# Kernel tuning notes

Measured on AMD Instinct MI355X. Metric: run time of the kernel, lower is better.

Reference implementation:

```python
import jax, jax.numpy as jnp
import numpy as np

B, L, E, H, T = 8, 4096, 512, 8, 2
D = E // H


def setup_inputs() -> dict:
    key = jax.random.key(0)
    ks = jax.random.split(key, 11)
    s = 0.02
    return {
        "query": jax.random.normal(ks[0], (B, L, E), jnp.float32),
        "key": jax.random.normal(ks[1], (B, L, E), jnp.float32),
        "value": jax.random.normal(ks[2], (B, L, E), jnp.float32),
        "Wq": jax.random.normal(ks[3], (T, E, E), jnp.float32) * s,
        "bq": jax.random.normal(ks[4], (T, E), jnp.float32) * s,
        "Wk": jax.random.normal(ks[5], (T, E, E), jnp.float32) * s,
        "bk": jax.random.normal(ks[6], (T, E), jnp.float32) * s,
        "Wv": jax.random.normal(ks[7], (E, E), jnp.float32) * s,
        "bv": jax.random.normal(ks[8], (E,), jnp.float32) * s,
        "Wout": jax.random.normal(ks[9], (E, E), jnp.float32) * s,
        "bout": jax.random.normal(ks[10], (E,), jnp.float32) * s,
    }


def reference(query, key, value, Wq, bq, Wk, bk, Wv, bv, Wout, bout):
    bsz, tgt_len, embed_dim = query.shape
    src_len = key.shape[1]
    n_head = H
    head_dim = embed_dim // n_head

    # value projection: (B,S,H,D)
    v = (value @ Wv.T + bv).reshape(bsz, src_len, n_head, head_dim)
    # faithful to torch: value.view(-1, bsz*n_head, head_dim).transpose(0,1)
    # WITHOUT permuting to (S,B,H,D) first -> pure memory reinterpretation
    v = jnp.swapaxes(v.reshape(src_len, bsz * n_head, head_dim), 0, 1)  # (BH,S,D)

    # per-term q/k projections -> (T,L,B,H,D) / (T,S,B,H,D)
    q = jnp.einsum('ble,tfe->tblf', query, Wq) + bq[:, None, None, :]
    k = jnp.einsum('bse,tfe->tbsf', key, Wk) + bk[:, None, None, :]
    q = q.reshape(T, bsz, tgt_len, n_head, head_dim).transpose(0, 2, 1, 3, 4)
    k = k.reshape(T, bsz, src_len, n_head, head_dim).transpose(0, 2, 1, 3, 4)

    # act_fun == softmax: q softmax over feature dim, k softmax over sequence dim (dim 0)
    q = jax.nn.softmax(q, axis=-1)
    k = jax.nn.softmax(k, axis=1)

    # flatten: (T, L, B*H, D) -> (T, B*H, L, D)
    q = jnp.swapaxes(q.reshape(T, tgt_len, bsz * n_head, head_dim), 1, 2)
    k = jnp.swapaxes(k.reshape(T, src_len, bsz * n_head, head_dim), 1, 2)

    # cosine positional reweighting (cosFormer): doubles feature dim
    m = max(src_len, tgt_len)
    idx = (np.pi / 2) * jnp.arange(1, m + 1, dtype=q.dtype) / m  # (m,)
    sin_q = jnp.sin(idx[:tgt_len])[None, None, :, None]
    cos_q = jnp.cos(idx[:tgt_len])[None, None, :, None]
    sin_k = jnp.sin(idx[:src_len])[None, None, :, None]
    cos_k = jnp.cos(idx[:src_len])[None, None, :, None]
    q = jnp.concatenate([q * sin_q, q * cos_q], axis=-1)  # (T,BH,L,2D)
    k = jnp.concatenate([k * sin_k, k * cos_k], axis=-1)  # (T,BH,S,2D)

    # linear attention: kv state then output, summed over terms
    kv = jnp.einsum('tnsd,nsm->tndm', k, v)          # (T,BH,2D,D)
    out = jnp.einsum('tnld,tndm->nlm', q, kv)        # (BH,L,D) summed over T

    # back to (B,L,E)
    out = jnp.swapaxes(out, 0, 1).reshape(tgt_len, bsz, embed_dim)
    out = jnp.swapaxes(out, 0, 1)
    return out @ Wout.T + bout
```

## Files before the change

### kernel.cpp

```cpp
#include <hip/hip_runtime.h>
#include <cstdio>

#define E_DIM 512
#define L_DIM 4096
#define B_DIM 8
#define H_DIM 8
#define T_DIM 2
#define M_ROWS 32768

typedef __attribute__((ext_vector_type(8))) __bf16 bf16x8;
typedef __attribute__((ext_vector_type(4))) float f32x4;

static __device__ __forceinline__ unsigned short f2bf(float f) {
  unsigned int u = __float_as_uint(f);
  return (unsigned short)((u + 0x7FFFu + ((u >> 16) & 1u)) >> 16);
}
static __device__ __forceinline__ unsigned int pkbf(float lo, float hi) {
  return (unsigned int)f2bf(lo) | ((unsigned int)f2bf(hi) << 16);
}
static __device__ __forceinline__ float bf2f(unsigned short u) {
  return __uint_as_float((unsigned int)u << 16);
}
static __device__ __forceinline__ void unpk8(uint4 u, float* f) {
  f[0] = bf2f((unsigned short)u.x); f[1] = bf2f((unsigned short)(u.x >> 16));
  f[2] = bf2f((unsigned short)u.y); f[3] = bf2f((unsigned short)(u.y >> 16));
  f[4] = bf2f((unsigned short)u.z); f[5] = bf2f((unsigned short)(u.z >> 16));
  f[6] = bf2f((unsigned short)u.w); f[7] = bf2f((unsigned short)(u.w >> 16));
}
static __device__ __forceinline__ int swz64(int row, int e) {
  return row * 64 + ((((e >> 3) ^ row) & 7) << 3) + (e & 7);
}
static __device__ __forceinline__ int swz128(int row, int e) {
  return row * 128 + ((((e >> 3) ^ row) & 7) << 3) + ((e >> 3) & 8) * 8 + (e & 7);
}
static __device__ __forceinline__ void gl_lds16(const unsigned short* g,
                                                unsigned short* l) {
  __builtin_amdgcn_global_load_lds(
      (const __attribute__((address_space(1))) unsigned int*)g,
      (__attribute__((address_space(3))) unsigned int*)l, 16, 0, 0);
}

__global__ void sincos_kernel(float* __restrict__ sintab, float* __restrict__ costab) {
  int i = blockIdx.x * blockDim.x + threadIdx.x;
  if (i < L_DIM) {
    float idx = 1.57079632679489662f * (float)(i + 1) / (float)L_DIM;
    sintab[i] = sinf(idx);
    costab[i] = cosf(idx);
  }
}

__global__ void convf2b(const float* __restrict__ src, unsigned short* __restrict__ dst,
                        int n8) {
  for (int i = blockIdx.x * blockDim.x + threadIdx.x; i < n8; i += gridDim.x * blockDim.x) {
    float4 a = *(const float4*)(src + (size_t)i * 8);
    float4 b = *(const float4*)(src + (size_t)i * 8 + 4);
    uint4 o;
    o.x = pkbf(a.x, a.y); o.y = pkbf(a.z, a.w);
    o.z = pkbf(b.x, b.y); o.w = pkbf(b.z, b.w);
    *(uint4*)(dst + (size_t)i * 8) = o;
  }
}

#define YHALF 16777216
template <bool OUTF32, bool STATS, int NBL2>
__global__ __launch_bounds__(256) void gemm_xwt(
    const unsigned short* __restrict__ X, const unsigned short* __restrict__ W,
    const float* __restrict__ bias, void* __restrict__ Yv,
    float* __restrict__ pmax, float* __restrict__ psum) {
  __shared__ __align__(16) unsigned short smem[32768];
  const int tid = threadIdx.x;
  const int id = blockIdx.x;
  const int j = id >> 3;
  const int mb = (id & 7) * 32 + (j >> NBL2);
  const int nb = j & ((1 << NBL2) - 1);
  const int m0 = mb * 128, n0 = nb * 128;
  const int lane = tid & 63;
  const int w = tid >> 6;
  const int wr = w >> 1, wc = w & 1;
  const int lr = lane & 15;
  const int lk = (lane >> 4) * 8;
  const int rq = lane >> 4;
  const int srow = lane >> 3;
  const int gsrc8 = ((lane & 7) ^ srow) * 8;
  f32x4 acc[4][4];
#pragma unroll
  for (int i = 0; i < 4; ++i)
#pragma unroll
    for (int jj = 0; jj < 4; ++jj) acc[i][jj] = (f32x4){0.f, 0.f, 0.f, 0.f};

#pragma unroll
  for (int i = 0; i < 4; ++i) {
    int rb = w * 32 + i * 8;
    gl_lds16(X + (size_t)(m0 + rb + srow) * 512 + gsrc8, &smem[rb * 64]);
    gl_lds16(W + (size_t)(n0 + rb + srow) * 512 + gsrc8, &smem[8192 + rb * 64]);
  }
  __syncthreads();

#pragma unroll
  for (int step = 0; step < 8; ++step) {
    const int cur = step & 1;
    if (step < 7) {
      unsigned short* Ab = smem + (cur ^ 1) * 16384;
      const int kn = (step + 1) * 64;
#pragma unroll
      for (int i = 0; i < 4; ++i) {
        int rb = w * 32 + i * 8;
        gl_lds16(X + (size_t)(m0 + rb + srow) * 512 + kn + gsrc8, &Ab[rb * 64]);
        gl_lds16(W + (size_t)(n0 + rb + srow) * 512 + kn + gsrc8,
                 &Ab[8192 + rb * 64]);
      }
    }
    const unsigned short* As = smem + cur * 16384;
    const unsigned short* Bs = As + 8192;
#pragma unroll
    for (int kk = 0; kk < 2; ++kk) {
      bf16x8 av[4], bv[4];
      int ke = kk * 32 + lk;
#pragma unroll
      for (int fm = 0; fm < 4; ++fm)
        av[fm] = *(const bf16x8*)&As[swz64(wr * 64 + fm * 16 + lr, ke)];
#pragma unroll
      for (int fn = 0; fn < 4; ++fn)
        bv[fn] = *(const bf16x8*)&Bs[swz64(wc * 64 + fn * 16 + lr, ke)];
#pragma unroll
      for (int fm = 0; fm < 4; ++fm)
#pragma unroll
        for (int fn = 0; fn < 4; ++fn)
          acc[fm][fn] = __builtin_amdgcn_mfma_f32_16x16x32_bf16(av[fm], bv[fn],
                                                                acc[fm][fn], 0, 0, 0);
    }
    __syncthreads();
  }

  if (STATS) {
    float* sf = (float*)smem;
#pragma unroll
    for (int fn = 0; fn < 4; ++fn) {
      float M = -3.0e38f;
#pragma unroll
      for (int fm = 0; fm < 4; ++fm)
#pragma unroll
        for (int jj = 0; jj < 4; ++jj) M = fmaxf(M, acc[fm][fn][jj]);
      M = fmaxf(M, __shfl_xor(M, 16));
      M = fmaxf(M, __shfl_xor(M, 32));
      float S = 0.f;
#pragma unroll
      for (int fm = 0; fm < 4; ++fm)
#pragma unroll
        for (int jj = 0; jj < 4; ++jj) S += __expf(acc[fm][fn][jj] - M);
      S += __shfl_xor(S, 16);
      S += __shfl_xor(S, 32);
      if (rq == 0) {
        int col = wc * 64 + fn * 16 + lr;
        sf[wr * 128 + col] = M;
        sf[256 + wr * 128 + col] = S;
      }
    }
    __syncthreads();
    if (tid < 128) {
      float M0 = sf[tid], M1 = sf[128 + tid];
      float S0 = sf[256 + tid], S1 = sf[384 + tid];
      float nm = fmaxf(M0, M1);
      float S = S0 * __expf(M0 - nm) + S1 * __expf(M1 - nm);
      int gc = n0 + tid;
      size_t mtile = (size_t)(m0 >> 7);
      pmax[mtile * (128 << NBL2) + gc] = nm + bias[gc];
      psum[mtile * (128 << NBL2) + gc] = S;
    }
    __syncthreads();
  }

  if (!OUTF32) {
    unsigned short* Cs = smem;
#pragma unroll
    for (int fn = 0; fn < 4; ++fn) {
      int col = wc * 64 + fn * 16 + lr;
      float bb = bias[n0 + col];
#pragma unroll
      for (int fm = 0; fm < 4; ++fm) {
        int row = wr * 64 + fm * 16 + rq * 4;
#pragma unroll
        for (int jj = 0; jj < 4; ++jj)
          Cs[(row + jj) * 136 + col] = f2bf(acc[fm][fn][jj] + bb);
      }
    }
    __syncthreads();
    unsigned short* Yb = (unsigned short*)Yv + (size_t)(n0 >> 9) * YHALF;
    const int nc = n0 & 511;
#pragma unroll
    for (int i = 0; i < 8; ++i) {
      int idx = tid + i * 256;
      int row = idx >> 4, g = idx & 15;
      *(uint4*)(Yb + (size_t)(m0 + row) * 512 + nc + g * 8) =
          *(const uint4*)&Cs[row * 136 + g * 8];
    }
  } else {
    float* Cf = (float*)smem;
    float* Yf = (float*)Yv;
#pragma unroll
    for (int p = 0; p < 2; ++p) {
      if (p) __syncthreads();
      if (wr == p) {
#pragma unroll
        for (int fn = 0; fn < 4; ++fn) {
          int col = wc * 64 + fn * 16 + lr;
          float bb = bias[n0 + col];
#pragma unroll
          for (int fm = 0; fm < 4; ++fm) {
            int lrow = fm * 16 + rq * 4;
#pragma unroll
            for (int jj = 0; jj < 4; ++jj)
              Cf[(lrow + jj) * 132 + col] = acc[fm][fn][jj] + bb;
          }
        }
      }
      __syncthreads();
#pragma unroll
      for (int i = 0; i < 8; ++i) {
        int idx = tid + i * 256;
        int row = idx >> 5, g = idx & 31;
        *(float4*)(Yf + (size_t)(m0 + p * 64 + row) * 512 + n0 + g * 4) =
            *(const float4*)&Cf[row * 132 + g * 4];
      }
    }
  }
}

__global__ void kcolstats_reduce(const float* __restrict__ pmax,
                                 const float* __restrict__ psum,
                                 float* __restrict__ colmax,
                                 float* __restrict__ colinv, int coloff) {
  int i = blockIdx.x * 256 + threadIdx.x;
  int b = i >> 9, f = i & 511;
  float M = -3.0e38f, S = 0.f;
#pragma unroll
  for (int c = 0; c < 32; ++c) {
    size_t mt = (size_t)(b * 32 + c);
    float m = pmax[mt * 1024 + coloff + f];
    float s = psum[mt * 1024 + coloff + f];
    float nm = fmaxf(M, m);
    S = S * __expf(M - nm) + s * __expf(m - nm);
    M = nm;
  }
  colmax[i] = M;
  colinv[i] = 1.f / S;
}

__global__ __launch_bounds__(256) void kv_mfma(
    const unsigned short* __restrict__ Kp, const unsigned short* __restrict__ Vpb,
    const float* __restrict__ colmax, const float* __restrict__ colinv,
    const float* __restrict__ sintab, const float* __restrict__ costab,
    float* __restrict__ kvpart) {
  __shared__ __align__(16) unsigned short kT[64 * 64];
  __shared__ __align__(16) unsigned short vT[128 * 64];
  __shared__ float cmaxs[64], cinvs[64];
  const int tid = threadIdx.x;
  const int chunk = blockIdx.x;
  const int n = blockIdx.y;
  const int b = n >> 3, h = n & 7;
  if (tid < 64) {
    cmaxs[tid] = colmax[b * E_DIM + h * 64 + tid];
    cinvs[tid] = colinv[b * E_DIM + h * 64 + tid];
  }
  const int lane = tid & 63;
  const int w = tid >> 6;
  const int lr = lane & 15;
  const int lk = (lane >> 4) * 8;
  const int sp = tid & 31;
  const int g = tid >> 5;
  f32x4 acc[4][2];
#pragma unroll
  for (int i = 0; i < 4; ++i) {
    acc[i][0] = (f32x4){0.f, 0.f, 0.f, 0.f};
    acc[i][1] = (f32x4){0.f, 0.f, 0.f, 0.f};
  }
  __syncthreads();

  for (int st = 0; st < 8; ++st) {
    int sA = chunk * 512 + st * 64 + 2 * sp;
    const unsigned short* kp = Kp + ((size_t)b * L_DIM + sA) * 512 + h * 64 + g * 8;
    uint4 ka = *(const uint4*)kp;
    uint4 kb = *(const uint4*)(kp + 512);
    int vr = ((sA >> 9) << 12) + ((sA & 511) << 3) + b;
    const unsigned short* vp = Vpb + (size_t)vr * 512 + h * 64 + g * 8;
    uint4 v0 = *(const uint4*)vp;
    uint4 v1 = *(const uint4*)(vp + 8 * 512);
    float kfa[8], kfb[8], vA[8], vB[8];
    unpk8(ka, kfa);
    unpk8(kb, kfb);
    unpk8(v0, vA);
    unpk8(v1, vB);
    float sS = sintab[sA], sC = costab[sA];
    float tS = sintab[sA + 1], tC = costab[sA + 1];
    __syncthreads();
#pragma unroll
    for (int i = 0; i < 8; ++i) {
      int d = g * 8 + i;
      float e0 = __expf(kfa[i] - cmaxs[d]) * cinvs[d];
      float e1 = __expf(kfb[i] - cmaxs[d]) * cinvs[d];
      *(unsigned int*)&kT[swz64(d, 2 * sp)] = pkbf(e0, e1);
    }
#pragma unroll
    for (int i = 0; i < 8; ++i) {
      int m = g * 8 + i;
      *(unsigned int*)&vT[swz64(m, 2 * sp)] = pkbf(vA[i] * sS, vB[i] * tS);
      *(unsigned int*)&vT[swz64(64 + m, 2 * sp)] = pkbf(vA[i] * sC, vB[i] * tC);
    }
    __syncthreads();
#pragma unroll
    for (int kk = 0; kk < 2; ++kk) {
      int ke = kk * 32 + lk;
      bf16x8 av[4], bv[2];
#pragma unroll
      for (int fm = 0; fm < 4; ++fm)
        av[fm] = *(const bf16x8*)&kT[swz64(fm * 16 + lr, ke)];
#pragma unroll
      for (int fn = 0; fn < 2; ++fn)
        bv[fn] = *(const bf16x8*)&vT[swz64(w * 32 + fn * 16 + lr, ke)];
#pragma unroll
      for (int fm = 0; fm < 4; ++fm)
#pragma unroll
        for (int fn = 0; fn < 2; ++fn)
          acc[fm][fn] = __builtin_amdgcn_mfma_f32_16x16x32_bf16(av[fm], bv[fn],
                                                                acc[fm][fn], 0, 0, 0);
    }
  }
  const int rq = lane >> 4;
#pragma unroll
  for (int fn = 0; fn < 2; ++fn) {
    int ncol = w * 32 + fn * 16 + lr;
    int m = ncol & 63;
    int ddbase = (ncol >> 6) * 64;
#pragma unroll
    for (int fm = 0; fm < 4; ++fm) {
#pragma unroll
      for (int jj = 0; jj < 4; ++jj) {
        int dd = ddbase + fm * 16 + rq * 4 + jj;
        kvpart[(((size_t)chunk * 64 + n) * 64 + m) * 128 + dd] = acc[fm][fn][jj];
      }
    }
  }
}

__global__ void kv_reduce_swz(const float* __restrict__ part,
                              unsigned short* __restrict__ kvT) {
  int i = blockIdx.x * 256 + threadIdx.x;
  float s = 0.f;
#pragma unroll
  for (int c = 0; c < 8; ++c) s += part[(size_t)c * 524288 + i];
  int dd = i & 127;
  int m = (i >> 7) & 63;
  int nm = i >> 7;
  int gg = dd >> 3;
  int e = ((gg & 8) | ((gg ^ m) & 7)) * 8 + (dd & 7);
  kvT[(size_t)nm * 128 + e] = f2bf(s);
}

__global__ __launch_bounds__(256) void out_fused(
    const unsigned short* __restrict__ Qp0, const unsigned short* __restrict__ Qp1,
    const unsigned short* __restrict__ kvT,
    const float* __restrict__ sintab, const float* __restrict__ costab,
    unsigned short* __restrict__ Yb) {
  __shared__ __align__(16) unsigned short q2s[64 * 128];
  __shared__ __align__(16) unsigned short kvs[2][64 * 128];
  const int tid = threadIdx.x;
  const int lc = blockIdx.x;
  const int n = blockIdx.y;
  const int b = n >> 3, h = n & 7;
  const int lane = tid & 63;
  const int w = tid >> 6;
  {
    const uint4* s0 = (const uint4*)(kvT + (size_t)n * 8192);
    const uint4* s1 = (const uint4*)(kvT + 524288 + (size_t)n * 8192);
    uint4* d0 = (uint4*)kvs[0];
    uint4* d1 = (uint4*)kvs[1];
#pragma unroll
    for (int i = 0; i < 4; ++i) {
      d0[tid + i * 256] = s0[tid + i * 256];
      d1[tid + i * 256] = s1[tid + i * 256];
    }
  }
  const int l0 = lc * 64;
  const int wr = w >> 1, wc = w & 1;
  const int lr = lane & 15;
  const int lk = (lane >> 4) * 8;
  const int rq = lane >> 4;
  f32x4 acc[2][2];
  acc[0][0] = acc[0][1] = acc[1][0] = acc[1][1] = (f32x4){0.f, 0.f, 0.f, 0.f};
#pragma unroll
  for (int t = 0; t < 2; ++t) {
    const unsigned short* Qp = t ? Qp1 : Qp0;
    if (t) __syncthreads();
#pragma unroll
    for (int i = 0; i < 2; ++i) {
      int idx = tid + i * 256;
      int row = idx >> 3;
      int g = idx & 7;
      uint4 q = *(const uint4*)(Qp + ((size_t)b * L_DIM + l0 + row) * 512 +
                                h * 64 + g * 8);
      float v[8];
      unpk8(q, v);
      float m8 = fmaxf(fmaxf(fmaxf(v[0], v[1]), fmaxf(v[2], v[3])),
                       fmaxf(fmaxf(v[4], v[5]), fmaxf(v[6], v[7])));
      m8 = fmaxf(m8, __shfl_xor(m8, 1));
      m8 = fmaxf(m8, __shfl_xor(m8, 2));
      m8 = fmaxf(m8, __shfl_xor(m8, 4));
      float e[8], s8;
#pragma unroll
      for (int k = 0; k < 8; ++k) e[k] = __expf(v[k] - m8);
      s8 = ((e[0] + e[1]) + (e[2] + e[3])) + ((e[4] + e[5]) + (e[6] + e[7]));
      s8 += __shfl_xor(s8, 1);
      s8 += __shfl_xor(s8, 2);
      s8 += __shfl_xor(s8, 4);
      float inv = 1.f / s8;
      int gl = l0 + row;
      float sn = sintab[gl] * inv;
      float cs = costab[gl] * inv;
      uint4 os, oc;
      os.x = pkbf(e[0] * sn, e[1] * sn); os.y = pkbf(e[2] * sn, e[3] * sn);
      os.z = pkbf(e[4] * sn, e[5] * sn); os.w = pkbf(e[6] * sn, e[7] * sn);
      oc.x = pkbf(e[0] * cs, e[1] * cs); oc.y = pkbf(e[2] * cs, e[3] * cs);
      oc.z = pkbf(e[4] * cs, e[5] * cs); oc.w = pkbf(e[6] * cs, e[7] * cs);
      *(uint4*)&q2s[swz128(row, g * 8)] = os;
      *(uint4*)&q2s[swz128(row, 64 + g * 8)] = oc;
    }
    __syncthreads();
#pragma unroll
    for (int ks = 0; ks < 4; ++ks) {
      int ke = ks * 32 + lk;
      bf16x8 av[2], bv[2];
#pragma unroll
      for (int fm = 0; fm < 2; ++fm)
        av[fm] = *(const bf16x8*)&q2s[swz128(wr * 32 + fm * 16 + lr, ke)];
#pragma unroll
      for (int fn = 0; fn < 2; ++fn)
        bv[fn] = *(const bf16x8*)&kvs[t][swz128(wc * 32 + fn * 16 + lr, ke)];
#pragma unroll
      for (int fm = 0; fm < 2; ++fm)
#pragma unroll
        for (int fn = 0; fn < 2; ++fn)
          acc[fm][fn] = __builtin_amdgcn_mfma_f32_16x16x32_bf16(av[fm], bv[fn],
                                                                acc[fm][fn], 0, 0, 0);
    }
  }
  __syncthreads();
  unsigned short* Os = q2s;
#pragma unroll
  for (int fn = 0; fn < 2; ++fn) {
    int col = wc * 32 + fn * 16 + lr;
#pragma unroll
    for (int fm = 0; fm < 2; ++fm) {
      int lrow = wr * 32 + fm * 16 + rq * 4;
#pragma unroll
      for (int jj = 0; jj < 4; ++jj)
        Os[(lrow + jj) * 72 + col] = f2bf(acc[fm][fn][jj]);
    }
  }
  __syncthreads();
#pragma unroll
  for (int i = 0; i < 2; ++i) {
    int idx = tid + i * 256;
    int row = idx >> 3, g = idx & 7;
    *(uint4*)(Yb + ((size_t)b * L_DIM + l0 + row) * 512 + h * 64 + g * 8) =
        *(const uint4*)&Os[row * 72 + g * 8];
  }
}

extern "C" void kernel_launch(void* const* d_in, const int* in_sizes, int n_in,
                              void* d_out, int out_size, void* d_ws, size_t ws_size,
                              hipStream_t stream) {
  const float* query = (const float*)d_in[0];
  const float* key   = (const float*)d_in[1];
  const float* value = (const float*)d_in[2];
  const float* Wq    = (const float*)d_in[3];
  const float* bq    = (const float*)d_in[4];
  const float* Wk    = (const float*)d_in[5];
  const float* bk    = (const float*)d_in[6];
  const float* Wv    = (const float*)d_in[7];
  const float* bv    = (const float*)d_in[8];
  const float* Wout  = (const float*)d_in[9];
  const float* bout  = (const float*)d_in[10];
  float* out = (float*)d_out;
  float* ws = (float*)d_ws;

  const size_t F_PROJ0 = 0;
  const size_t F_PROJ1 = F_PROJ0 + 8388608;
  const size_t F_VPB   = F_PROJ1 + 8388608;
  const size_t F_KVP   = F_VPB + 8388608;
  const size_t F_KVT   = F_KVP + 4194304;
  const size_t F_XBUF  = F_KVT + 524288;
  const size_t F_WBF   = F_XBUF + 8388608;
  const size_t F_CMAX  = F_WBF + 786432;
  const size_t F_CINV  = F_CMAX + 8192;
  const size_t F_SIN   = F_CINV + 8192;
  const size_t F_COS   = F_SIN + 4096;
  const size_t TOTALF  = F_COS + 4096;
  if (ws_size < TOTALF * sizeof(float)) {
    fprintf(stderr, "kernel_launch: ws too small (%zu < %zu)\n", ws_size, TOTALF * 4);
    return;
  }
  unsigned short* proj0 = (unsigned short*)(ws + F_PROJ0);
  unsigned short* vpb   = (unsigned short*)(ws + F_VPB);
  float* kvpart = ws + F_KVP;
  unsigned short* kvT  = (unsigned short*)(ws + F_KVT);
  unsigned short* xbuf = (unsigned short*)(ws + F_XBUF);
  unsigned short* wbf  = (unsigned short*)(ws + F_WBF);
  float* cmax = ws + F_CMAX;
  float* cinv = ws + F_CINV;
  float* sintab = ws + F_SIN;
  float* costab = ws + F_COS;
  float* pmax = kvpart;
  float* psum = kvpart + 262144;
  const size_t WQ_O = 0, WK_O = 524288, WV_O = 1048576, WOUT_O = 1310720;

  sincos_kernel<<<16, 256, 0, stream>>>(sintab, costab);
  convf2b<<<256, 256, 0, stream>>>(Wq, wbf + WQ_O, 65536);
  convf2b<<<256, 256, 0, stream>>>(Wk, wbf + WK_O, 65536);
  convf2b<<<128, 256, 0, stream>>>(Wv, wbf + WV_O, 32768);
  convf2b<<<128, 256, 0, stream>>>(Wout, wbf + WOUT_O, 32768);

  convf2b<<<2048, 256, 0, stream>>>(value, xbuf, 2097152);
  gemm_xwt<false, false, 2><<<1024, 256, 0, stream>>>(xbuf, wbf + WV_O, bv, vpb,
                                                      nullptr, nullptr);

  convf2b<<<2048, 256, 0, stream>>>(key, xbuf, 2097152);
  gemm_xwt<false, true, 3><<<2048, 256, 0, stream>>>(xbuf, wbf + WK_O, bk, proj0,
                                                     pmax, psum);
  kcolstats_reduce<<<16, 256, 0, stream>>>(pmax, psum, cmax, cinv, 0);
  kcolstats_reduce<<<16, 256, 0, stream>>>(pmax, psum, cmax + 4096, cinv + 4096, 512);
  for (int t = 0; t < T_DIM; ++t) {
    unsigned short* projt = proj0 + (size_t)t * YHALF;
    kv_mfma<<<dim3(8, 64), 256, 0, stream>>>(projt, vpb, cmax + t * 4096,
                                             cinv + t * 4096, sintab, costab,
                                             kvpart);
    kv_reduce_swz<<<2048, 256, 0, stream>>>(kvpart, kvT + (size_t)t * 524288);
  }

  convf2b<<<2048, 256, 0, stream>>>(query, xbuf, 2097152);
  gemm_xwt<false, false, 3><<<2048, 256, 0, stream>>>(xbuf, wbf + WQ_O, bq, proj0,
                                                      nullptr, nullptr);
  out_fused<<<dim3(64, 64), 256, 0, stream>>>(proj0, proj0 + YHALF, kvT,
                                              sintab, costab, xbuf);
  gemm_xwt<true, false, 2><<<1024, 256, 0, stream>>>(xbuf, wbf + WOUT_O, bout, out,
                                                     nullptr, nullptr);
}
```

Baseline: 325.8 us.

## Fuse key softmax and KV-state accumulation into key projection GEMM epilogue

```diff
diff --git a/kernel.cpp b/kernel.cpp
--- a/kernel.cpp
+++ b/kernel.cpp
@@ -62,12 +62,15 @@
 }
 
 #define YHALF 16777216
-template <bool OUTF32, bool STATS, int NBL2>
+template <int MODE, int NBL2>
 __global__ __launch_bounds__(256) void gemm_xwt(
     const unsigned short* __restrict__ X, const unsigned short* __restrict__ W,
     const float* __restrict__ bias, void* __restrict__ Yv,
-    float* __restrict__ pmax, float* __restrict__ psum) {
+    const unsigned short* __restrict__ Vpb, const float* __restrict__ sintab,
+    const float* __restrict__ costab, float* __restrict__ kvglob,
+    float* __restrict__ Ssum) {
   __shared__ __align__(16) unsigned short smem[32768];
+  __shared__ float sf2[256];
   const int tid = threadIdx.x;
   const int id = blockIdx.x;
   const int j = id >> 3;
@@ -132,45 +135,122 @@
     __syncthreads();
   }
 
-  if (STATS) {
-    float* sf = (float*)smem;
+  if (MODE == 2) {
+    const int b_idx = m0 >> 12;
+    const int l0 = m0 & 4095;
+    const int t = n0 >> 9;
+    const int h_base = (n0 & 511) >> 6;
+    unsigned short* eT = smem;
+    unsigned short* vT = smem + 16384;
 #pragma unroll
     for (int fn = 0; fn < 4; ++fn) {
-      float M = -3.0e38f;
-#pragma unroll
-      for (int fm = 0; fm < 4; ++fm)
-#pragma unroll
-        for (int jj = 0; jj < 4; ++jj) M = fmaxf(M, acc[fm][fn][jj]);
-      M = fmaxf(M, __shfl_xor(M, 16));
-      M = fmaxf(M, __shfl_xor(M, 32));
+      int col = wc * 64 + fn * 16 + lr;
+      float bb = bias[n0 + col];
       float S = 0.f;
 #pragma unroll
-      for (int fm = 0; fm < 4; ++fm)
-#pragma unroll
-        for (int jj = 0; jj < 4; ++jj) S += __expf(acc[fm][fn][jj] - M);
+      for (int fm = 0; fm < 4; ++fm) {
+        float e0 = __expf(acc[fm][fn][0] + bb);
+        float e1 = __expf(acc[fm][fn][1] + bb);
+        float e2 = __expf(acc[fm][fn][2] + bb);
+        float e3 = __expf(acc[fm][fn][3] + bb);
+        S += (e0 + e1) + (e2 + e3);
+        int srow0 = wr * 64 + fm * 16 + rq * 4;
+        *(unsigned int*)&eT[swz128(col, srow0)] = pkbf(e0, e1);
+        *(unsigned int*)&eT[swz128(col, srow0 + 2)] = pkbf(e2, e3);
+      }
       S += __shfl_xor(S, 16);
       S += __shfl_xor(S, 32);
-      if (rq == 0) {
-        int col = wc * 64 + fn * 16 + lr;
-        sf[wr * 128 + col] = M;
-        sf[256 + wr * 128 + col] = S;
+      if (rq == 0) sf2[wr * 128 + col] = S;
+    }
+#pragma unroll
+    for (int rep = 0; rep < 2; ++rep) {
+      int tt = tid + rep * 256;
+      int g = tt >> 6;
+      int sp = tt & 63;
+      int s0 = 2 * sp;
+      int sg = l0 + s0;
+      int vrow = ((sg >> 9) << 12) + ((sg & 511) << 3) + b_idx;
+      const unsigned short* vp = Vpb + (size_t)vrow * 512 + h_base * 64 + g * 8;
+      uint4 v0 = *(const uint4*)vp;
+      uint4 v1 = *(const uint4*)(vp + 8 * 512);
+      float vA[8], vB[8];
+      unpk8(v0, vA);
+      unpk8(v1, vB);
+      float sn0 = sintab[sg], cs0 = costab[sg];
+      float sn1 = sintab[sg + 1], cs1 = costab[sg + 1];
+#pragma unroll
+      for (int i = 0; i < 8; ++i) {
+        int m = g * 8 + i;
+        *(unsigned int*)&vT[swz128(m, s0)] = pkbf(vA[i] * sn0, vB[i] * sn1);
+        *(unsigned int*)&vT[swz128(64 + m, s0)] = pkbf(vA[i] * cs0, vB[i] * cs1);
       }
     }
     __syncthreads();
     if (tid < 128) {
-      float M0 = sf[tid], M1 = sf[128 + tid];
-      float S0 = sf[256 + tid], S1 = sf[384 + tid];
-      float nm = fmaxf(M0, M1);
-      float S = S0 * __expf(M0 - nm) + S1 * __expf(M1 - nm);
-      int gc = n0 + tid;
-      size_t mtile = (size_t)(m0 >> 7);
-      pmax[mtile * (128 << NBL2) + gc] = nm + bias[gc];
-      psum[mtile * (128 << NBL2) + gc] = S;
-    }
-    __syncthreads();
-  }
-
-  if (!OUTF32) {
+      float S = sf2[tid] + sf2[128 + tid];
+      atomicAdd(&Ssum[t * 4096 + b_idx * 512 + (n0 & 511) + tid], S);
+    }
+#pragma unroll
+    for (int h = 0; h < 2; ++h) {
+      if (h == 1) {
+        __syncthreads();
+#pragma unroll
+        for (int rep = 0; rep < 2; ++rep) {
+          int tt = tid + rep * 256;
+          int g = tt >> 6;
+          int sp = tt & 63;
+          int s0 = 2 * sp;
+          int sg = l0 + s0;
+          int vrow = ((sg >> 9) << 12) + ((sg & 511) << 3) + b_idx;
+          const unsigned short* vp =
+              Vpb + (size_t)vrow * 512 + (h_base + 1) * 64 + g * 8;
+          uint4 v0 = *(const uint4*)vp;
+          uint4 v1 = *(const uint4*)(vp + 8 * 512);
+          float vA[8], vB[8];
+          unpk8(v0, vA);
+          unpk8(v1, vB);
+          float sn0 = sintab[sg], cs0 = costab[sg];
+          float sn1 = sintab[sg + 1], cs1 = costab[sg + 1];
+#pragma unroll
+          for (int i = 0; i < 8; ++i) {
+            int m = g * 8 + i;
+            *(unsigned int*)&vT[swz128(m, s0)] = pkbf(vA[i] * sn0, vB[i] * sn1);
+            *(unsigned int*)&vT[swz128(64 + m, s0)] = pkbf(vA[i] * cs0, vB[i] * cs1);
+          }
+        }
+        __syncthreads();
+      }
+      f32x4 acc2[8];
+#pragma unroll
+      for (int fn = 0; fn < 8; ++fn) acc2[fn] = (f32x4){0.f, 0.f, 0.f, 0.f};
+#pragma unroll
+      for (int ks = 0; ks < 4; ++ks) {
+        int ke = ks * 32 + lk;
+        bf16x8 av = *(const bf16x8*)&eT[swz128(h * 64 + w * 16 + lr, ke)];
+#pragma unroll
+        for (int fn = 0; fn < 8; ++fn) {
+          bf16x8 bv = *(const bf16x8*)&vT[swz128(fn * 16 + lr, ke)];
+          acc2[fn] = __builtin_amdgcn_mfma_f32_16x16x32_bf16(av, bv, acc2[fn], 0, 0, 0);
+        }
+      }
+      int n_kv = b_idx * 8 + h_base + h;
+      float* kvn = kvglob + ((size_t)t * 64 + n_kv) * 8192;
+#pragma unroll
+      for (int fn = 0; fn < 8; ++fn) {
+        int mm = fn * 16 + lr;
+        int m = mm & 63;
+        int ddhalf = (mm >> 6) * 64;
+#pragma unroll
+        for (int jj = 0; jj < 4; ++jj) {
+          int dd = ddhalf + w * 16 + rq * 4 + jj;
+          atomicAdd(&kvn[m * 128 + dd], acc2[fn][jj]);
+        }
+      }
+    }
+    return;
+  }
+
+  if (MODE == 0) {
     unsigned short* Cs = smem;
 #pragma unroll
     for (int fn = 0; fn < 4; ++fn) {
@@ -226,134 +306,19 @@
   }
 }
 
-__global__ void kcolstats_reduce(const float* __restrict__ pmax,
-                                 const float* __restrict__ psum,
-                                 float* __restrict__ colmax,
-                                 float* __restrict__ colinv, int coloff) {
+__global__ void kv_norm(const float* __restrict__ kvglob,
+                        const float* __restrict__ Ssum,
+                        unsigned short* __restrict__ kvT) {
   int i = blockIdx.x * 256 + threadIdx.x;
-  int b = i >> 9, f = i & 511;
-  float M = -3.0e38f, S = 0.f;
-#pragma unroll
-  for (int c = 0; c < 32; ++c) {
-    size_t mt = (size_t)(b * 32 + c);
-    float m = pmax[mt * 1024 + coloff + f];
-    float s = psum[mt * 1024 + coloff + f];
-    float nm = fmaxf(M, m);
-    S = S * __expf(M - nm) + s * __expf(m - nm);
-    M = nm;
-  }
-  colmax[i] = M;
-  colinv[i] = 1.f / S;
-}
-
-__global__ __launch_bounds__(256) void kv_mfma(
-    const unsigned short* __restrict__ Kp, const unsigned short* __restrict__ Vpb,
-    const float* __restrict__ colmax, const float* __restrict__ colinv,
-    const float* __restrict__ sintab, const float* __restrict__ costab,
-    float* __restrict__ kvpart) {
-  __shared__ __align__(16) unsigned short kT[64 * 64];
-  __shared__ __align__(16) unsigned short vT[128 * 64];
-  __shared__ float cmaxs[64], cinvs[64];
-  const int tid = threadIdx.x;
-  const int chunk = blockIdx.x;
-  const int n = blockIdx.y;
-  const int b = n >> 3, h = n & 7;
-  if (tid < 64) {
-    cmaxs[tid] = colmax[b * E_DIM + h * 64 + tid];
-    cinvs[tid] = colinv[b * E_DIM + h * 64 + tid];
-  }
-  const int lane = tid & 63;
-  const int w = tid >> 6;
-  const int lr = lane & 15;
-  const int lk = (lane >> 4) * 8;
-  const int sp = tid & 31;
-  const int g = tid >> 5;
-  f32x4 acc[4][2];
-#pragma unroll
-  for (int i = 0; i < 4; ++i) {
-    acc[i][0] = (f32x4){0.f, 0.f, 0.f, 0.f};
-    acc[i][1] = (f32x4){0.f, 0.f, 0.f, 0.f};
-  }
-  __syncthreads();
-
-  for (int st = 0; st < 8; ++st) {
-    int sA = chunk * 512 + st * 64 + 2 * sp;
-    const unsigned short* kp = Kp + ((size_t)b * L_DIM + sA) * 512 + h * 64 + g * 8;
-    uint4 ka = *(const uint4*)kp;
-    uint4 kb = *(const uint4*)(kp + 512);
-    int vr = ((sA >> 9) << 12) + ((sA & 511) << 3) + b;
-    const unsigned short* vp = Vpb + (size_t)vr * 512 + h * 64 + g * 8;
-    uint4 v0 = *(const uint4*)vp;
-    uint4 v1 = *(const uint4*)(vp + 8 * 512);
-    float kfa[8], kfb[8], vA[8], vB[8];
-    unpk8(ka, kfa);
-    unpk8(kb, kfb);
-    unpk8(v0, vA);
-    unpk8(v1, vB);
-    float sS = sintab[sA], sC = costab[sA];
-    float tS = sintab[sA + 1], tC = costab[sA + 1];
-    __syncthreads();
-#pragma unroll
-    for (int i = 0; i < 8; ++i) {
-      int d = g * 8 + i;
-      float e0 = __expf(kfa[i] - cmaxs[d]) * cinvs[d];
-      float e1 = __expf(kfb[i] - cmaxs[d]) * cinvs[d];
-      *(unsigned int*)&kT[swz64(d, 2 * sp)] = pkbf(e0, e1);
-    }
-#pragma unroll
-    for (int i = 0; i < 8; ++i) {
-      int m = g * 8 + i;
-      *(unsigned int*)&vT[swz64(m, 2 * sp)] = pkbf(vA[i] * sS, vB[i] * tS);
-      *(unsigned int*)&vT[swz64(64 + m, 2 * sp)] = pkbf(vA[i] * sC, vB[i] * tC);
-    }
-    __syncthreads();
-#pragma unroll
-    for (int kk = 0; kk < 2; ++kk) {
-      int ke = kk * 32 + lk;
-      bf16x8 av[4], bv[2];
-#pragma unroll
-      for (int fm = 0; fm < 4; ++fm)
-        av[fm] = *(const bf16x8*)&kT[swz64(fm * 16 + lr, ke)];
-#pragma unroll
-      for (int fn = 0; fn < 2; ++fn)
-        bv[fn] = *(const bf16x8*)&vT[swz64(w * 32 + fn * 16 + lr, ke)];
-#pragma unroll
-      for (int fm = 0; fm < 4; ++fm)
-#pragma unroll
-        for (int fn = 0; fn < 2; ++fn)
-          acc[fm][fn] = __builtin_amdgcn_mfma_f32_16x16x32_bf16(av[fm], bv[fn],
-                                                                acc[fm][fn], 0, 0, 0);
-    }
-  }
-  const int rq = lane >> 4;
-#pragma unroll
-  for (int fn = 0; fn < 2; ++fn) {
-    int ncol = w * 32 + fn * 16 + lr;
-    int m = ncol & 63;
-    int ddbase = (ncol >> 6) * 64;
-#pragma unroll
-    for (int fm = 0; fm < 4; ++fm) {
-#pragma unroll
-      for (int jj = 0; jj < 4; ++jj) {
-        int dd = ddbase + fm * 16 + rq * 4 + jj;
-        kvpart[(((size_t)chunk * 64 + n) * 64 + m) * 128 + dd] = acc[fm][fn][jj];
-      }
-    }
-  }
-}
-
-__global__ void kv_reduce_swz(const float* __restrict__ part,
-                              unsigned short* __restrict__ kvT) {
-  int i = blockIdx.x * 256 + threadIdx.x;
-  float s = 0.f;
-#pragma unroll
-  for (int c = 0; c < 8; ++c) s += part[(size_t)c * 524288 + i];
   int dd = i & 127;
   int m = (i >> 7) & 63;
-  int nm = i >> 7;
+  int n = (i >> 13) & 63;
+  int t = i >> 19;
+  float S = Ssum[t * 4096 + (n >> 3) * 512 + (n & 7) * 64 + (dd & 63)];
+  float v = kvglob[i] / S;
   int gg = dd >> 3;
   int e = ((gg & 8) | ((gg ^ m) & 7)) * 8 + (dd & 7);
-  kvT[(size_t)nm * 128 + e] = f2bf(s);
+  kvT[(size_t)t * 524288 + (((i >> 7) & 4095) << 7) + e] = f2bf(v);
 }
 
 __global__ __launch_bounds__(256) void out_fused(
@@ -486,13 +451,12 @@
   const size_t F_PROJ0 = 0;
   const size_t F_PROJ1 = F_PROJ0 + 8388608;
   const size_t F_VPB   = F_PROJ1 + 8388608;
-  const size_t F_KVP   = F_VPB + 8388608;
-  const size_t F_KVT   = F_KVP + 4194304;
+  const size_t F_KVG   = F_VPB + 8388608;
+  const size_t F_KVT   = F_KVG + 4194304;
   const size_t F_XBUF  = F_KVT + 524288;
   const size_t F_WBF   = F_XBUF + 8388608;
-  const size_t F_CMAX  = F_WBF + 786432;
-  const size_t F_CINV  = F_CMAX + 8192;
-  const size_t F_SIN   = F_CINV + 8192;
+  const size_t F_SSUM  = F_WBF + 786432;
+  const size_t F_SIN   = F_SSUM + 8192;
   const size_t F_COS   = F_SIN + 4096;
   const size_t TOTALF  = F_COS + 4096;
   if (ws_size < TOTALF * sizeof(float)) {
@@ -501,16 +465,13 @@
   }
   unsigned short* proj0 = (unsigned short*)(ws + F_PROJ0);
   unsigned short* vpb   = (unsigned short*)(ws + F_VPB);
-  float* kvpart = ws + F_KVP;
+  float* kvglob = ws + F_KVG;
   unsigned short* kvT  = (unsigned short*)(ws + F_KVT);
   unsigned short* xbuf = (unsigned short*)(ws + F_XBUF);
   unsigned short* wbf  = (unsigned short*)(ws + F_WBF);
-  float* cmax = ws + F_CMAX;
-  float* cinv = ws + F_CINV;
+  float* Ssum = ws + F_SSUM;
   float* sintab = ws + F_SIN;
   float* costab = ws + F_COS;
-  float* pmax = kvpart;
-  float* psum = kvpart + 262144;
   const size_t WQ_O = 0, WK_O = 524288, WV_O = 1048576, WOUT_O = 1310720;
 
   sincos_kernel<<<16, 256, 0, stream>>>(sintab, costab);
@@ -520,27 +481,24 @@
   convf2b<<<128, 256, 0, stream>>>(Wout, wbf + WOUT_O, 32768);
 
   convf2b<<<2048, 256, 0, stream>>>(value, xbuf, 2097152);
-  gemm_xwt<false, false, 2><<<1024, 256, 0, stream>>>(xbuf, wbf + WV_O, bv, vpb,
-                                                      nullptr, nullptr);
-
+  gemm_xwt<0, 2><<<1024, 256, 0, stream>>>(xbuf, wbf + WV_O, bv, vpb,
+                                           nullptr, nullptr, nullptr, nullptr,
+                                           nullptr);
+
+  hipMemsetAsync(kvglob, 0, 4194304, stream);
+  hipMemsetAsync(Ssum, 0, 32768, stream);
   convf2b<<<2048, 256, 0, stream>>>(key, xbuf, 2097152);
-  gemm_xwt<false, true, 3><<<2048, 256, 0, stream>>>(xbuf, wbf + WK_O, bk, proj0,
-                                                     pmax, psum);
-  kcolstats_reduce<<<16, 256, 0, stream>>>(pmax, psum, cmax, cinv, 0);
-  kcolstats_reduce<<<16, 256, 0, stream>>>(pmax, psum, cmax + 4096, cinv + 4096, 512);
-  for (int t = 0; t < T_DIM; ++t) {
-    unsigned short* projt = proj0 + (size_t)t * YHALF;
-    kv_mfma<<<dim3(8, 64), 256, 0, stream>>>(projt, vpb, cmax + t * 4096,
-                                             cinv + t * 4096, sintab, costab,
-                                             kvpart);
-    kv_reduce_swz<<<2048, 256, 0, stream>>>(kvpart, kvT + (size_t)t * 524288);
-  }
+  gemm_xwt<2, 3><<<2048, 256, 0, stream>>>(xbuf, wbf + WK_O, bk, nullptr,
+                                           vpb, sintab, costab, kvglob, Ssum);
+  kv_norm<<<4096, 256, 0, stream>>>(kvglob, Ssum, kvT);
 
   convf2b<<<2048, 256, 0, stream>>>(query, xbuf, 2097152);
-  gemm_xwt<false, false, 3><<<2048, 256, 0, stream>>>(xbuf, wbf + WQ_O, bq, proj0,
-                                                      nullptr, nullptr);
+  gemm_xwt<0, 3><<<2048, 256, 0, stream>>>(xbuf, wbf + WQ_O, bq, proj0,
+                                           nullptr, nullptr, nullptr, nullptr,
+                                           nullptr);
   out_fused<<<dim3(64, 64), 256, 0, stream>>>(proj0, proj0 + YHALF, kvT,
                                               sintab, costab, xbuf);
-  gemm_xwt<true, false, 2><<<1024, 256, 0, stream>>>(xbuf, wbf + WOUT_O, bout, out,
-                                                     nullptr, nullptr);
-}
+  gemm_xwt<1, 2><<<1024, 256, 0, stream>>>(xbuf, wbf + WOUT_O, bout, out,
+                                           nullptr, nullptr, nullptr, nullptr,
+                                           nullptr);
+}
```

New measurement: 670.7 us. 2.06x slower.

## Fuse q/k softmax into projection GEMM epilogues and defer key normalization

Applied to the files above, without the earlier changes.

```diff
diff --git a/kernel.cpp b/kernel.cpp
--- a/kernel.cpp
+++ b/kernel.cpp
@@ -62,12 +62,13 @@
 }
 
 #define YHALF 16777216
-template <bool OUTF32, bool STATS, int NBL2>
+template <int MODE, int NBL2>
 __global__ __launch_bounds__(256) void gemm_xwt(
     const unsigned short* __restrict__ X, const unsigned short* __restrict__ W,
     const float* __restrict__ bias, void* __restrict__ Yv,
-    float* __restrict__ pmax, float* __restrict__ psum) {
+    float* __restrict__ psum) {
   __shared__ __align__(16) unsigned short smem[32768];
+  __shared__ float sf2[256];
   const int tid = threadIdx.x;
   const int id = blockIdx.x;
   const int j = id >> 3;
@@ -132,59 +133,78 @@
     __syncthreads();
   }
 
-  if (STATS) {
-    float* sf = (float*)smem;
-#pragma unroll
-    for (int fn = 0; fn < 4; ++fn) {
-      float M = -3.0e38f;
-#pragma unroll
-      for (int fm = 0; fm < 4; ++fm)
-#pragma unroll
-        for (int jj = 0; jj < 4; ++jj) M = fmaxf(M, acc[fm][fn][jj]);
-      M = fmaxf(M, __shfl_xor(M, 16));
-      M = fmaxf(M, __shfl_xor(M, 32));
-      float S = 0.f;
-#pragma unroll
-      for (int fm = 0; fm < 4; ++fm)
-#pragma unroll
-        for (int jj = 0; jj < 4; ++jj) S += __expf(acc[fm][fn][jj] - M);
-      S += __shfl_xor(S, 16);
-      S += __shfl_xor(S, 32);
-      if (rq == 0) {
+  if (MODE == 0 || MODE == 2 || MODE == 3) {
+    unsigned short* Cs = smem;
+    if (MODE == 0) {
+#pragma unroll
+      for (int fn = 0; fn < 4; ++fn) {
         int col = wc * 64 + fn * 16 + lr;
-        sf[wr * 128 + col] = M;
-        sf[256 + wr * 128 + col] = S;
+        float bb = bias[n0 + col];
+#pragma unroll
+        for (int fm = 0; fm < 4; ++fm) {
+          int row = wr * 64 + fm * 16 + rq * 4;
+#pragma unroll
+          for (int jj = 0; jj < 4; ++jj)
+            Cs[(row + jj) * 136 + col] = f2bf(acc[fm][fn][jj] + bb);
+        }
+      }
+    } else if (MODE == 2) {
+#pragma unroll
+      for (int fn = 0; fn < 4; ++fn) {
+        int col = wc * 64 + fn * 16 + lr;
+        float bb = bias[n0 + col];
+        float S = 0.f;
+#pragma unroll
+        for (int fm = 0; fm < 4; ++fm) {
+          int row = wr * 64 + fm * 16 + rq * 4;
+#pragma unroll
+          for (int jj = 0; jj < 4; ++jj) {
+            float u = __expf(acc[fm][fn][jj] + bb);
+            S += u;
+            Cs[(row + jj) * 136 + col] = f2bf(u);
+          }
+        }
+        S += __shfl_xor(S, 16);
+        S += __shfl_xor(S, 32);
+        if (rq == 0) sf2[wr * 128 + col] = S;
+      }
+    } else {
+      float bb[4];
+#pragma unroll
+      for (int fn = 0; fn < 4; ++fn) bb[fn] = bias[n0 + wc * 64 + fn * 16 + lr];
+#pragma unroll
+      for (int fm = 0; fm < 4; ++fm) {
+#pragma unroll
+        for (int jj = 0; jj < 4; ++jj) {
+          float v[4];
+#pragma unroll
+          for (int fn = 0; fn < 4; ++fn) v[fn] = acc[fm][fn][jj] + bb[fn];
+          float m = fmaxf(fmaxf(v[0], v[1]), fmaxf(v[2], v[3]));
+          m = fmaxf(m, __shfl_xor(m, 1));
+          m = fmaxf(m, __shfl_xor(m, 2));
+          m = fmaxf(m, __shfl_xor(m, 4));
+          m = fmaxf(m, __shfl_xor(m, 8));
+          float e[4];
+          float s = 0.f;
+#pragma unroll
+          for (int fn = 0; fn < 4; ++fn) { e[fn] = __expf(v[fn] - m); s += e[fn]; }
+          s += __shfl_xor(s, 1);
+          s += __shfl_xor(s, 2);
+          s += __shfl_xor(s, 4);
+          s += __shfl_xor(s, 8);
+          float inv = 1.f / s;
+          int row = wr * 64 + fm * 16 + rq * 4 + jj;
+#pragma unroll
+          for (int fn = 0; fn < 4; ++fn)
+            Cs[row * 136 + wc * 64 + fn * 16 + lr] = f2bf(e[fn] * inv);
+        }
       }
     }
     __syncthreads();
-    if (tid < 128) {
-      float M0 = sf[tid], M1 = sf[128 + tid];
-      float S0 = sf[256 + tid], S1 = sf[384 + tid];
-      float nm = fmaxf(M0, M1);
-      float S = S0 * __expf(M0 - nm) + S1 * __expf(M1 - nm);
-      int gc = n0 + tid;
-      size_t mtile = (size_t)(m0 >> 7);
-      pmax[mtile * (128 << NBL2) + gc] = nm + bias[gc];
-      psum[mtile * (128 << NBL2) + gc] = S;
-    }
-    __syncthreads();
-  }
-
-  if (!OUTF32) {
-    unsigned short* Cs = smem;
-#pragma unroll
-    for (int fn = 0; fn < 4; ++fn) {
-      int col = wc * 64 + fn * 16 + lr;
-      float bb = bias[n0 + col];
-#pragma unroll
-      for (int fm = 0; fm < 4; ++fm) {
-        int row = wr * 64 + fm * 16 + rq * 4;
-#pragma unroll
-        for (int jj = 0; jj < 4; ++jj)
-          Cs[(row + jj) * 136 + col] = f2bf(acc[fm][fn][jj] + bb);
-      }
-    }
-    __syncthreads();
+    if (MODE == 2 && tid < 128) {
+      float S = sf2[tid] + sf2[128 + tid];
+      psum[(size_t)(m0 >> 7) * (128 << NBL2) + n0 + tid] = S;
+    }
     unsigned short* Yb = (unsigned short*)Yv + (size_t)(n0 >> 9) * YHALF;
     const int nc = n0 & 511;
 #pragma unroll
@@ -226,42 +246,27 @@
   }
 }
 
-__global__ void kcolstats_reduce(const float* __restrict__ pmax,
-                                 const float* __restrict__ psum,
-                                 float* __restrict__ colmax,
-                                 float* __restrict__ colinv, int coloff) {
+__global__ void colsum_reduce(const float* __restrict__ psum,
+                              float* __restrict__ colinv, int coloff) {
   int i = blockIdx.x * 256 + threadIdx.x;
   int b = i >> 9, f = i & 511;
-  float M = -3.0e38f, S = 0.f;
-#pragma unroll
-  for (int c = 0; c < 32; ++c) {
-    size_t mt = (size_t)(b * 32 + c);
-    float m = pmax[mt * 1024 + coloff + f];
-    float s = psum[mt * 1024 + coloff + f];
-    float nm = fmaxf(M, m);
-    S = S * __expf(M - nm) + s * __expf(m - nm);
-    M = nm;
-  }
-  colmax[i] = M;
+  float S = 0.f;
+#pragma unroll
+  for (int c = 0; c < 32; ++c)
+    S += psum[(size_t)(b * 32 + c) * 1024 + coloff + f];
   colinv[i] = 1.f / S;
 }
 
 __global__ __launch_bounds__(256) void kv_mfma(
-    const unsigned short* __restrict__ Kp, const unsigned short* __restrict__ Vpb,
-    const float* __restrict__ colmax, const float* __restrict__ colinv,
+    const unsigned short* __restrict__ Up, const unsigned short* __restrict__ Vpb,
     const float* __restrict__ sintab, const float* __restrict__ costab,
     float* __restrict__ kvpart) {
   __shared__ __align__(16) unsigned short kT[64 * 64];
   __shared__ __align__(16) unsigned short vT[128 * 64];
-  __shared__ float cmaxs[64], cinvs[64];
   const int tid = threadIdx.x;
   const int chunk = blockIdx.x;
   const int n = blockIdx.y;
   const int b = n >> 3, h = n & 7;
-  if (tid < 64) {
-    cmaxs[tid] = colmax[b * E_DIM + h * 64 + tid];
-    cinvs[tid] = colinv[b * E_DIM + h * 64 + tid];
-  }
   const int lane = tid & 63;
   const int w = tid >> 6;
   const int lr = lane & 15;
@@ -274,20 +279,20 @@
     acc[i][0] = (f32x4){0.f, 0.f, 0.f, 0.f};
     acc[i][1] = (f32x4){0.f, 0.f, 0.f, 0.f};
   }
-  __syncthreads();
 
   for (int st = 0; st < 8; ++st) {
     int sA = chunk * 512 + st * 64 + 2 * sp;
-    const unsigned short* kp = Kp + ((size_t)b * L_DIM + sA) * 512 + h * 64 + g * 8;
+    const unsigned short* kp = Up + ((size_t)b * L_DIM + sA) * 512 + h * 64 + g * 8;
     uint4 ka = *(const uint4*)kp;
     uint4 kb = *(const uint4*)(kp + 512);
     int vr = ((sA >> 9) << 12) + ((sA & 511) << 3) + b;
     const unsigned short* vp = Vpb + (size_t)vr * 512 + h * 64 + g * 8;
     uint4 v0 = *(const uint4*)vp;
     uint4 v1 = *(const uint4*)(vp + 8 * 512);
-    float kfa[8], kfb[8], vA[8], vB[8];
-    unpk8(ka, kfa);
-    unpk8(kb, kfb);
+    unsigned short ua[8], ub[8];
+    *(uint4*)ua = ka;
+    *(uint4*)ub = kb;
+    float vA[8], vB[8];
     unpk8(v0, vA);
     unpk8(v1, vB);
     float sS = sintab[sA], sC = costab[sA];
@@ -296,9 +301,8 @@
 #pragma unroll
     for (int i = 0; i < 8; ++i) {
       int d = g * 8 + i;
-      float e0 = __expf(kfa[i] - cmaxs[d]) * cinvs[d];
-      float e1 = __expf(kfb[i] - cmaxs[d]) * cinvs[d];
-      *(unsigned int*)&kT[swz64(d, 2 * sp)] = pkbf(e0, e1);
+      *(unsigned int*)&kT[swz64(d, 2 * sp)] =
+          (unsigned int)ua[i] | ((unsigned int)ub[i] << 16);
     }
 #pragma unroll
     for (int i = 0; i < 8; ++i) {
@@ -343,6 +347,7 @@
 }
 
 __global__ void kv_reduce_swz(const float* __restrict__ part,
+                              const float* __restrict__ colinv,
                               unsigned short* __restrict__ kvT) {
   int i = blockIdx.x * 256 + threadIdx.x;
   float s = 0.f;
@@ -350,14 +355,15 @@
   for (int c = 0; c < 8; ++c) s += part[(size_t)c * 524288 + i];
   int dd = i & 127;
   int m = (i >> 7) & 63;
-  int nm = i >> 7;
+  int n = i >> 13;
+  float sc = colinv[(n >> 3) * 512 + (n & 7) * 64 + (dd & 63)];
   int gg = dd >> 3;
   int e = ((gg & 8) | ((gg ^ m) & 7)) * 8 + (dd & 7);
-  kvT[(size_t)nm * 128 + e] = f2bf(s);
+  kvT[(size_t)(i >> 7) * 128 + e] = f2bf(s * sc);
 }
 
 __global__ __launch_bounds__(256) void out_fused(
-    const unsigned short* __restrict__ Qp0, const unsigned short* __restrict__ Qp1,
+    const unsigned short* __restrict__ Pp0, const unsigned short* __restrict__ Pp1,
     const unsigned short* __restrict__ kvT,
     const float* __restrict__ sintab, const float* __restrict__ costab,
     unsigned short* __restrict__ Yb) {
@@ -389,38 +395,25 @@
   acc[0][0] = acc[0][1] = acc[1][0] = acc[1][1] = (f32x4){0.f, 0.f, 0.f, 0.f};
 #pragma unroll
   for (int t = 0; t < 2; ++t) {
-    const unsigned short* Qp = t ? Qp1 : Qp0;
+    const unsigned short* Pp = t ? Pp1 : Pp0;
     if (t) __syncthreads();
 #pragma unroll
     for (int i = 0; i < 2; ++i) {
       int idx = tid + i * 256;
       int row = idx >> 3;
       int g = idx & 7;
-      uint4 q = *(const uint4*)(Qp + ((size_t)b * L_DIM + l0 + row) * 512 +
+      uint4 q = *(const uint4*)(Pp + ((size_t)b * L_DIM + l0 + row) * 512 +
                                 h * 64 + g * 8);
       float v[8];
       unpk8(q, v);
-      float m8 = fmaxf(fmaxf(fmaxf(v[0], v[1]), fmaxf(v[2], v[3])),
-                       fmaxf(fmaxf(v[4], v[5]), fmaxf(v[6], v[7])));
-      m8 = fmaxf(m8, __shfl_xor(m8, 1));
-      m8 = fmaxf(m8, __shfl_xor(m8, 2));
-      m8 = fmaxf(m8, __shfl_xor(m8, 4));
-      float e[8], s8;
-#pragma unroll
-      for (int k = 0; k < 8; ++k) e[k] = __expf(v[k] - m8);
-      s8 = ((e[0] + e[1]) + (e[2] + e[3])) + ((e[4] + e[5]) + (e[6] + e[7]));
-      s8 += __shfl_xor(s8, 1);
-      s8 += __shfl_xor(s8, 2);
-      s8 += __shfl_xor(s8, 4);
-      float inv = 1.f / s8;
       int gl = l0 + row;
-      float sn = sintab[gl] * inv;
-      float cs = costab[gl] * inv;
+      float sn = sintab[gl];
+      float cs = costab[gl];
       uint4 os, oc;
-      os.x = pkbf(e[0] * sn, e[1] * sn); os.y = pkbf(e[2] * sn, e[3] * sn);
-      os.z = pkbf(e[4] * sn, e[5] * sn); os.w = pkbf(e[6] * sn, e[7] * sn);
-      oc.x = pkbf(e[0] * cs, e[1] * cs); oc.y = pkbf(e[2] * cs, e[3] * cs);
-      oc.z = pkbf(e[4] * cs, e[5] * cs); oc.w = pkbf(e[6] * cs, e[7] * cs);
+      os.x = pkbf(v[0] * sn, v[1] * sn); os.y = pkbf(v[2] * sn, v[3] * sn);
+      os.z = pkbf(v[4] * sn, v[5] * sn); os.w = pkbf(v[6] * sn, v[7] * sn);
+      oc.x = pkbf(v[0] * cs, v[1] * cs); oc.y = pkbf(v[2] * cs, v[3] * cs);
+      oc.z = pkbf(v[4] * cs, v[5] * cs); oc.w = pkbf(v[6] * cs, v[7] * cs);
       *(uint4*)&q2s[swz128(row, g * 8)] = os;
       *(uint4*)&q2s[swz128(row, 64 + g * 8)] = oc;
     }
@@ -490,8 +483,7 @@
   const size_t F_KVT   = F_KVP + 4194304;
   const size_t F_XBUF  = F_KVT + 524288;
   const size_t F_WBF   = F_XBUF + 8388608;
-  const size_t F_CMAX  = F_WBF + 786432;
-  const size_t F_CINV  = F_CMAX + 8192;
+  const size_t F_CINV  = F_WBF + 786432;
   const size_t F_SIN   = F_CINV + 8192;
   const size_t F_COS   = F_SIN + 4096;
   const size_t TOTALF  = F_COS + 4096;
@@ -505,12 +497,10 @@
   unsigned short* kvT  = (unsigned short*)(ws + F_KVT);
   unsigned short* xbuf = (unsigned short*)(ws + F_XBUF);
   unsigned short* wbf  = (unsigned short*)(ws + F_WBF);
-  float* cmax = ws + F_CMAX;
   float* cinv = ws + F_CINV;
   float* sintab = ws + F_SIN;
   float* costab = ws + F_COS;
-  float* pmax = kvpart;
-  float* psum = kvpart + 262144;
+  float* psum = kvpart;
   const size_t WQ_O = 0, WK_O = 524288, WV_O = 1048576, WOUT_O = 1310720;
 
   sincos_kernel<<<16, 256, 0, stream>>>(sintab, costab);
@@ -520,27 +510,22 @@
   convf2b<<<128, 256, 0, stream>>>(Wout, wbf + WOUT_O, 32768);
 
   convf2b<<<2048, 256, 0, stream>>>(value, xbuf, 2097152);
-  gemm_xwt<false, false, 2><<<1024, 256, 0, stream>>>(xbuf, wbf + WV_O, bv, vpb,
-                                                      nullptr, nullptr);
+  gemm_xwt<0, 2><<<1024, 256, 0, stream>>>(xbuf, wbf + WV_O, bv, vpb, nullptr);
 
   convf2b<<<2048, 256, 0, stream>>>(key, xbuf, 2097152);
-  gemm_xwt<false, true, 3><<<2048, 256, 0, stream>>>(xbuf, wbf + WK_O, bk, proj0,
-                                                     pmax, psum);
-  kcolstats_reduce<<<16, 256, 0, stream>>>(pmax, psum, cmax, cinv, 0);
-  kcolstats_reduce<<<16, 256, 0, stream>>>(pmax, psum, cmax + 4096, cinv + 4096, 512);
+  gemm_xwt<2, 3><<<2048, 256, 0, stream>>>(xbuf, wbf + WK_O, bk, proj0, psum);
+  colsum_reduce<<<16, 256, 0, stream>>>(psum, cinv, 0);
+  colsum_reduce<<<16, 256, 0, stream>>>(psum, cinv + 4096, 512);
   for (int t = 0; t < T_DIM; ++t) {
     unsigned short* projt = proj0 + (size_t)t * YHALF;
-    kv_mfma<<<dim3(8, 64), 256, 0, stream>>>(projt, vpb, cmax + t * 4096,
-                                             cinv + t * 4096, sintab, costab,
-                                             kvpart);
-    kv_reduce_swz<<<2048, 256, 0, stream>>>(kvpart, kvT + (size_t)t * 524288);
+    kv_mfma<<<dim3(8, 64), 256, 0, stream>>>(projt, vpb, sintab, costab, kvpart);
+    kv_reduce_swz<<<2048, 256, 0, stream>>>(kvpart, cinv + t * 4096,
+                                            kvT + (size_t)t * 524288);
   }
 
   convf2b<<<2048, 256, 0, stream>>>(query, xbuf, 2097152);
-  gemm_xwt<false, false, 3><<<2048, 256, 0, stream>>>(xbuf, wbf + WQ_O, bq, proj0,
-                                                      nullptr, nullptr);
+  gemm_xwt<3, 3><<<2048, 256, 0, stream>>>(xbuf, wbf + WQ_O, bq, proj0, nullptr);
   out_fused<<<dim3(64, 64), 256, 0, stream>>>(proj0, proj0 + YHALF, kvT,
                                               sintab, costab, xbuf);
-  gemm_xwt<true, false, 2><<<1024, 256, 0, stream>>>(xbuf, wbf + WOUT_O, bout, out,
-                                                     nullptr, nullptr);
-}
+  gemm_xwt<1, 2><<<1024, 256, 0, stream>>>(xbuf, wbf + WOUT_O, bout, out, nullptr);
+}
```

Result: slower. 338.3 us (+3.8%).
